# Kernel tuning notes

Measured on AMD Instinct MI355X. Metric: run time of the kernel, lower is better.

## Reference

```python
import jax, jax.numpy as jnp
import numpy as np

N = 8192          # tokens
CD = 512          # coarse_dim
FD = 512          # fine_dim
CB = 4096         # coarse codebook size
FB = 8192         # fine codebook size
COST = 0.25       # commitment cost
LRELU = 0.1
EPS = 1e-5


def _vq(x, emb):
    # squared-distance cdist: [n, K]
    d = jnp.sum(x * x, axis=1, keepdims=True) + jnp.sum(emb * emb, axis=1) - 2.0 * (x @ emb.T)
    idx = jnp.argmin(d, axis=1)          # temperature=1.0 (updates=0); scaling doesn't change argmin
    q = emb[idx]                          # gather == one-hot @ emb, without materializing one-hot
    e_loss = jnp.mean((jax.lax.stop_gradient(q) - x) ** 2)
    q_loss = jnp.mean((q - jax.lax.stop_gradient(x)) ** 2)
    loss = q_loss + COST * e_loss
    q_st = x + jax.lax.stop_gradient(q - x)   # straight-through
    return q_st, loss


def _mlp(x, w, b, g, be):
    # Linear (torch: x @ W.T + b) -> LayerNorm -> LeakyReLU(0.1)
    h = x @ w.T + b
    m = jnp.mean(h, axis=-1, keepdims=True)
    v = jnp.var(h, axis=-1, keepdims=True)
    h = (h - m) / jnp.sqrt(v + EPS) * g + be
    return jnp.where(h > 0, h, LRELU * h)


def setup_inputs() -> dict:
    key = jax.random.key(0)
    ks = jax.random.split(key, 6)
    xav_c = float(np.sqrt(6.0 / (CB + CD)))
    xav_f = float(np.sqrt(6.0 / (FB + FD)))
    lin_s = float(np.sqrt(1.0 / CD))
    return {
        'z': jax.random.normal(ks[0], (N, CD + FD), dtype=jnp.float32),
        'coarse_emb': jax.random.uniform(ks[1], (CB, CD), jnp.float32, -xav_c, xav_c),
        'fine_emb': jax.random.uniform(ks[2], (FB, FD), jnp.float32, -xav_f, xav_f),
        'w_c2f': jax.random.uniform(ks[3], (FD, CD), jnp.float32, -lin_s, lin_s),
        'b_c2f': jnp.zeros((FD,), jnp.float32),
        'g_c2f': jnp.ones((FD,), jnp.float32),
        'be_c2f': jnp.zeros((FD,), jnp.float32),
        'w_f2c': jax.random.uniform(ks[4], (CD, FD), jnp.float32, -lin_s, lin_s),
        'b_f2c': jnp.zeros((CD,), jnp.float32),
        'g_f2c': jnp.ones((CD,), jnp.float32),
        'be_f2c': jnp.zeros((CD,), jnp.float32),
        'gate_c_raw': jnp.float32(0.5),
        'gate_f_raw': jnp.float32(0.5),
    }


def reference(z, coarse_emb, fine_emb, w_c2f, b_c2f, g_c2f, be_c2f,
              w_f2c, b_f2c, g_f2c, be_f2c, gate_c_raw, gate_f_raw):
    split = z.shape[1] // 2
    z_coarse, z_fine = z[:, :split], z[:, split:]

    z_coarse_q, coarse_loss = _vq(z_coarse, coarse_emb)
    coarse_influence = _mlp(jax.lax.stop_gradient(z_coarse_q), w_c2f, b_c2f, g_c2f, be_c2f)
    gate_c = jax.nn.sigmoid(gate_c_raw)

    residual = z_fine - gate_c * coarse_influence
    z_fine_q, fine_loss = _vq(residual, fine_emb)

    fine_feedback = _mlp(jax.lax.stop_gradient(z_fine_q), w_f2c, b_f2c, g_f2c, be_f2c)
    gate_f = jax.nn.sigmoid(gate_f_raw)

    z_coarse_corrected = z_coarse_q + 0.1 * gate_f * fine_feedback
    z_fine_reconstructed = z_fine_q + gate_c * coarse_influence
    z_hierarchical = jnp.concatenate([z_coarse_corrected, z_fine_reconstructed], axis=1)
    vq_loss = coarse_loss + fine_loss
    return z_hierarchical, vq_loss
```

## Files before the change

kernel.cpp:

```cpp
#include <hip/hip_runtime.h>
#include <hip/hip_bf16.h>
#include <cstdint>
#include <cstddef>

#define KD 512

#define OFF_CN   0u
#define OFF_FN   16384u
#define OFF_ZN   49152u
#define OFF_RN   81920u
#define OFF_LOSS 114688u
#define OFF_AMC  114944u
#define OFF_AMF  180480u
#define OFF_CEH  246016u
#define OFF_CEL  4440320u
#define OFF_FEH  8634624u
#define OFF_FEL  17023232u
#define OFF_ZCH  25411840u
#define OFF_ZCL  33800448u
#define OFF_RH   42189056u
#define OFF_RL   50577664u
#define OFF_W1H  58966272u
#define OFF_W1L  59490560u
#define OFF_W2H  60014848u
#define OFF_W2L  60539136u
#define OFF_H    61063424u
#define OFF_INFL 77840640u


typedef __attribute__((ext_vector_type(8))) short bf16x8;
typedef __attribute__((ext_vector_type(4))) float f32x4;

__device__ __forceinline__ bf16x8 as_bf16x8(int4 v) {
  union { int4 i; bf16x8 b; } u; u.i = v; return u.b;
}

__device__ __forceinline__ void gl_lds16(const void* g, void* l) {
  __builtin_amdgcn_global_load_lds(
      (const __attribute__((address_space(1))) void*)g,
      (__attribute__((address_space(3))) void*)l, 16, 0, 0);
}

__device__ __forceinline__ float block_sum(float v, float* sred) {
#pragma unroll
  for (int off = 32; off > 0; off >>= 1) v += __shfl_down(v, off, 64);
  if ((threadIdx.x & 63) == 0) sred[threadIdx.x >> 6] = v;
  __syncthreads();
  float r = sred[0] + sred[1] + sred[2] + sred[3];
  __syncthreads();
  return r;
}

__device__ __forceinline__ float sigmoidf_(float x) { return 1.0f / (1.0f + expf(-x)); }

__device__ __forceinline__ void split_bf16(float v, __hip_bfloat16* hi, __hip_bfloat16* lo) {
  __hip_bfloat16 h = __float2bfloat16(v);
  *hi = h;
  *lo = __float2bfloat16(v - __bfloat162float(h));
}

__global__ __launch_bounds__(256) void prep(
    const float* __restrict__ ce, const float* __restrict__ fe, const float* __restrict__ z,
    const float* __restrict__ w1, const float* __restrict__ w2,
    float* __restrict__ cn, float* __restrict__ fn, float* __restrict__ zn,
    __hip_bfloat16* __restrict__ ceH, __hip_bfloat16* __restrict__ ceL,
    __hip_bfloat16* __restrict__ feH, __hip_bfloat16* __restrict__ feL,
    __hip_bfloat16* __restrict__ zcH, __hip_bfloat16* __restrict__ zcL,
    __hip_bfloat16* __restrict__ w1H, __hip_bfloat16* __restrict__ w1L,
    __hip_bfloat16* __restrict__ w2H, __hip_bfloat16* __restrict__ w2L,
    float* __restrict__ lossp) {
  __shared__ float sred[4];
  const int b = blockIdx.x, t = threadIdx.x;
  const float* src;
  float* nd = nullptr;
  __hip_bfloat16 *dh, *dl;
  int fragMode = 0;
  size_t row;
  if (b < 4096) {
    row = b; src = ce + row * KD; nd = cn + row; dh = ceH; dl = ceL; fragMode = 1;
  } else if (b < 12288) {
    row = b - 4096; src = fe + row * KD; nd = fn + row; dh = feH; dl = feL; fragMode = 1;
  } else if (b < 20480) {
    row = b - 12288; src = z + row * 1024; nd = zn + row; dh = zcH; dl = zcL;
  } else if (b < 20992) {
    row = b - 20480; src = w1 + row * KD; dh = w1H; dl = w1L;
  } else {
    row = b - 20992; src = w2 + row * KD; dh = w2H; dl = w2L;
  }
  float acc = 0.0f;
  if (fragMode) {
    float v0 = src[t], v1 = src[t + 256];
    acc = v0 * v0 + v1 * v1;
  } else {
#pragma unroll
    for (int j = 0; j < 2; ++j) {
      int c = t + j * 256;
      float v = src[c];
      acc += v * v;
      __hip_bfloat16 h, l;
      split_bf16(v, &h, &l);
      dh[row * KD + c] = h;
      dl[row * KD + c] = l;
    }
  }
  if (nd) {
    float s = block_sum(acc, sred);
    if (t == 0) nd[0] = s;
  } else {
    __syncthreads();
    __syncthreads();
  }
  if (fragMode && t < 64) {
    union { int4 i; __hip_bfloat16 s[8]; } ph, pl;
#pragma unroll
    for (int j = 0; j < 8; ++j) {
      float v = src[8 * t + j];
      split_bf16(v, &ph.s[j], &pl.s[j]);
    }
    const int chunkIdx = (int)(((row >> 4) * 16 + (t >> 2)) * 64 +
                               ((size_t)((t & 3) << 4) | (row & 15)));
    ((int4*)dh)[chunkIdx] = ph.i;
    ((int4*)dl)[chunkIdx] = pl.i;
  }
  if (b == 20480 && t == 0) lossp[0] = 0.0f;
}

__global__ __launch_bounds__(256) void vq7(
    const int4* __restrict__ AfH, const int4* __restrict__ AfL,
    const __hip_bfloat16* __restrict__ Bh, const __hip_bfloat16* __restrict__ Bl,
    const float* __restrict__ qn, const float* __restrict__ cn,
    unsigned long long* __restrict__ amin) {
  __shared__ __align__(16) __hip_bfloat16 sBh[3][128 * 32];
  __shared__ __align__(16) __hip_bfloat16 sBl[3][128 * 32];
  const int t = threadIdx.x;
  const int w = t >> 6, l = t & 63;
  const int rowTile = blockIdx.y << 7;
  const int colTile = blockIdx.x << 7;
  const int wr = (w >> 1) << 6;
  const int wc = (w & 1) << 6;

  const int rl = l >> 2;
  const int sbp = (l & 3) ^ ((l >> 3) & 3);
  const size_t gOff0 = (size_t)(colTile + (w << 5) + rl) * KD + (sbp << 3);
  const size_t gOff1 = gOff0 + (size_t)16 * KD;
  const int lOff0 = (w << 5) << 5;
  const int lOff1 = lOff0 + (16 << 5);

  const int fr = l & 15;
  const int q = l >> 4;

  int aB[4];
#pragma unroll
  for (int mt = 0; mt < 4; ++mt)
    aB[mt] = (((rowTile + wr + (mt << 4)) >> 4) << 10) + l;

  f32x4 acc[4][4];
#pragma unroll
  for (int i = 0; i < 4; ++i)
#pragma unroll
    for (int j = 0; j < 4; ++j) acc[i][j] = (f32x4){0.f, 0.f, 0.f, 0.f};

#define STAGE_B(bi, ck) do {                                      \
    gl_lds16(Bh + gOff0 + ((size_t)(ck) << 5), &sBh[bi][lOff0]);  \
    gl_lds16(Bh + gOff1 + ((size_t)(ck) << 5), &sBh[bi][lOff1]);  \
    gl_lds16(Bl + gOff0 + ((size_t)(ck) << 5), &sBl[bi][lOff0]);  \
    gl_lds16(Bl + gOff1 + ((size_t)(ck) << 5), &sBl[bi][lOff1]);  \
  } while (0)

  int4 aH[4], aL[4];
  STAGE_B(0, 0);
  STAGE_B(1, 1);
#pragma unroll
  for (int mt = 0; mt < 4; ++mt) { aH[mt] = AfH[aB[mt]]; aL[mt] = AfL[aB[mt]]; }
  __builtin_amdgcn_sched_barrier(0);
  asm volatile("s_waitcnt vmcnt(0)" ::: "memory");

#pragma unroll
  for (int i = 0; i < 16; ++i) {
    __builtin_amdgcn_s_barrier();
    __builtin_amdgcn_sched_barrier(0);
    if (i + 2 < 16) STAGE_B((i + 2) % 3, i + 2);
    __builtin_amdgcn_sched_barrier(0);

    bf16x8 afh[4], afl[4];
#pragma unroll
    for (int mt = 0; mt < 4; ++mt) {
      afh[mt] = as_bf16x8(aH[mt]);
      afl[mt] = as_bf16x8(aL[mt]);
    }
    if (i + 1 < 16) {
#pragma unroll
      for (int mt = 0; mt < 4; ++mt) {
        aH[mt] = AfH[aB[mt] + ((i + 1) << 6)];
        aL[mt] = AfL[aB[mt] + ((i + 1) << 6)];
      }
    }
    __builtin_amdgcn_sched_barrier(0);

    __builtin_amdgcn_s_setprio(1);
    const int cb = i % 3;
    bf16x8 bfh[4], bfl[4];
#pragma unroll
    for (int nt = 0; nt < 4; ++nt) {
      const int rB = wc + (nt << 4) + fr;
      const int o = (rB << 5) + ((q ^ ((rB >> 1) & 3)) << 3);
      bfh[nt] = *(const bf16x8*)(sBh[cb] + o);
      bfl[nt] = *(const bf16x8*)(sBl[cb] + o);
    }
#pragma unroll
    for (int mt = 0; mt < 4; ++mt)
#pragma unroll
      for (int nt = 0; nt < 4; ++nt) {
        acc[mt][nt] = __builtin_amdgcn_mfma_f32_16x16x32_bf16(afh[mt], bfh[nt], acc[mt][nt], 0, 0, 0);
        acc[mt][nt] = __builtin_amdgcn_mfma_f32_16x16x32_bf16(afh[mt], bfl[nt], acc[mt][nt], 0, 0, 0);
        acc[mt][nt] = __builtin_amdgcn_mfma_f32_16x16x32_bf16(afl[mt], bfh[nt], acc[mt][nt], 0, 0, 0);
      }
    __builtin_amdgcn_s_setprio(0);
  }

#pragma unroll
  for (int nt = 0; nt < 4; ++nt) {
    const int query = colTile + wc + (nt << 4) + fr;
    const float xn = qn[query];
    unsigned long long key = ~0ULL;
#pragma unroll
    for (int mt = 0; mt < 4; ++mt) {
#pragma unroll
      for (int reg = 0; reg < 4; ++reg) {
        const int code = rowTile + wr + (mt << 4) + (q << 2) + reg;
        float d = (xn + cn[code]) - 2.0f * acc[mt][nt][reg];
        unsigned ub = __float_as_uint(d);
        ub = (ub & 0x80000000u) ? ~ub : (ub | 0x80000000u);
        unsigned long long k2 = ((unsigned long long)ub << 32) | (unsigned long long)(unsigned)code;
        if (k2 < key) key = k2;
      }
    }
    unsigned long long o1 = __shfl_xor(key, 16, 64);
    if (o1 < key) key = o1;
    unsigned long long o2 = __shfl_xor(key, 32, 64);
    if (o2 < key) key = o2;
    if (l < 16) atomicMin(amin + colTile + wc + (nt << 4) + l, key);
  }
}

__global__ __launch_bounds__(256) void mlp6(
    const int4* __restrict__ AfH, const int4* __restrict__ AfL,
    const unsigned long long* __restrict__ gather,
    const __hip_bfloat16* __restrict__ Bh, const __hip_bfloat16* __restrict__ Bl,
    const float* __restrict__ bias, float* __restrict__ C) {
  __shared__ __align__(16) __hip_bfloat16 sAh[128 * 32];
  __shared__ __align__(16) __hip_bfloat16 sAl[128 * 32];
  __shared__ __align__(16) __hip_bfloat16 sBh[128 * 32];
  __shared__ __align__(16) __hip_bfloat16 sBl[128 * 32];
  const int t = threadIdx.x;
  const int w = t >> 6, l = t & 63;
  const int rowTile = blockIdx.y << 7;
  const int colTile = blockIdx.x << 7;
  const int wr = (w >> 1) << 6;
  const int wc = (w & 1) << 6;

  const int srow = t >> 2;
  const int sb = t & 3;
  const int skE = sb << 3;
  const int swz = (sb ^ ((srow >> 1) & 3)) << 3;
  const int wOff0 = (srow << 5) + swz;
  const int wOff1 = ((srow + 64) << 5) + swz;

  unsigned i0 = ((const unsigned*)gather)[2 * (rowTile + srow)];
  unsigned i1 = ((const unsigned*)gather)[2 * (rowTile + 64 + srow)];
  const int a0 = (int)((i0 >> 4) << 10) + (sb << 4) + (int)(i0 & 15);
  const int a1 = (int)((i1 >> 4) << 10) + (sb << 4) + (int)(i1 & 15);
  const size_t br0 = (size_t)(colTile + srow) * KD;
  const size_t br1 = (size_t)(colTile + 64 + srow) * KD;

  const int fr = l & 15;
  const int q = l >> 4;

  f32x4 acc[4][4];
#pragma unroll
  for (int i = 0; i < 4; ++i)
#pragma unroll
    for (int j = 0; j < 4; ++j) acc[i][j] = (f32x4){0.f, 0.f, 0.f, 0.f};

  for (int kk = 0; kk < KD; kk += 32) {
    const int kc64 = (kk >> 5) << 6;
    int4 vAh0 = AfH[a0 + kc64];
    int4 vAh1 = AfH[a1 + kc64];
    int4 vAl0 = AfL[a0 + kc64];
    int4 vAl1 = AfL[a1 + kc64];
    int4 vBh0 = *(const int4*)(Bh + br0 + kk + skE);
    int4 vBh1 = *(const int4*)(Bh + br1 + kk + skE);
    int4 vBl0 = *(const int4*)(Bl + br0 + kk + skE);
    int4 vBl1 = *(const int4*)(Bl + br1 + kk + skE);
    __syncthreads();
    *(int4*)(sAh + wOff0) = vAh0; *(int4*)(sAh + wOff1) = vAh1;
    *(int4*)(sAl + wOff0) = vAl0; *(int4*)(sAl + wOff1) = vAl1;
    *(int4*)(sBh + wOff0) = vBh0; *(int4*)(sBh + wOff1) = vBh1;
    *(int4*)(sBl + wOff0) = vBl0; *(int4*)(sBl + wOff1) = vBl1;
    __syncthreads();

    bf16x8 afh[4], afl[4], bfh[4], bfl[4];
#pragma unroll
    for (int mt = 0; mt < 4; ++mt) {
      const int rA = wr + (mt << 4) + fr;
      const int o = (rA << 5) + ((q ^ ((rA >> 1) & 3)) << 3);
      afh[mt] = *(const bf16x8*)(sAh + o);
      afl[mt] = *(const bf16x8*)(sAl + o);
    }
#pragma unroll
    for (int nt = 0; nt < 4; ++nt) {
      const int rB = wc + (nt << 4) + fr;
      const int o = (rB << 5) + ((q ^ ((rB >> 1) & 3)) << 3);
      bfh[nt] = *(const bf16x8*)(sBh + o);
      bfl[nt] = *(const bf16x8*)(sBl + o);
    }
#pragma unroll
    for (int mt = 0; mt < 4; ++mt)
#pragma unroll
      for (int nt = 0; nt < 4; ++nt) {
        acc[mt][nt] = __builtin_amdgcn_mfma_f32_16x16x32_bf16(afh[mt], bfh[nt], acc[mt][nt], 0, 0, 0);
        acc[mt][nt] = __builtin_amdgcn_mfma_f32_16x16x32_bf16(afh[mt], bfl[nt], acc[mt][nt], 0, 0, 0);
        acc[mt][nt] = __builtin_amdgcn_mfma_f32_16x16x32_bf16(afl[mt], bfh[nt], acc[mt][nt], 0, 0, 0);
      }
  }

  const int quad = l >> 4;
#pragma unroll
  for (int mt = 0; mt < 4; ++mt) {
#pragma unroll
    for (int reg = 0; reg < 4; ++reg) {
      const int row = rowTile + wr + (mt << 4) + (quad << 2) + reg;
#pragma unroll
      for (int nt = 0; nt < 4; ++nt) {
        const int col = colTile + wc + (nt << 4) + fr;
        C[(size_t)row * KD + col] = acc[mt][nt][reg] + bias[col];
      }
    }
  }
}

__global__ __launch_bounds__(256) void ln_residual(
    const float* __restrict__ h, const float* __restrict__ g, const float* __restrict__ be,
    const float* __restrict__ z, const float* __restrict__ gRaw,
    __hip_bfloat16* __restrict__ infl, float* __restrict__ rn,
    __hip_bfloat16* __restrict__ rH, __hip_bfloat16* __restrict__ rL) {
  __shared__ float sred[4];
  const int row = blockIdx.x, t = threadIdx.x;
  const size_t base = (size_t)row * KD;
  float h0 = h[base + t], h1 = h[base + t + 256];
  float m = block_sum(h0 + h1, sred) * (1.0f / 512.0f);
  float d0 = h0 - m, d1 = h1 - m;
  float var = block_sum(d0 * d0 + d1 * d1, sred) * (1.0f / 512.0f);
  float sq = sqrtf(var + 1e-5f);
  float gc = sigmoidf_(gRaw[0]);
  float v0 = d0 / sq * g[t] + be[t];
  float v1 = d1 / sq * g[t + 256] + be[t + 256];
  v0 = v0 > 0.0f ? v0 : 0.1f * v0;
  v1 = v1 > 0.0f ? v1 : 0.1f * v1;
  infl[base + t] = __float2bfloat16(v0);
  infl[base + t + 256] = __float2bfloat16(v1);
  float zf0 = z[(size_t)row * 1024 + 512 + t];
  float zf1 = z[(size_t)row * 1024 + 512 + t + 256];
  float r0 = zf0 - gc * v0, r1 = zf1 - gc * v1;
  __hip_bfloat16 hh, ll;
  split_bf16(r0, &hh, &ll);
  rH[base + t] = hh; rL[base + t] = ll;
  split_bf16(r1, &hh, &ll);
  rH[base + t + 256] = hh; rL[base + t + 256] = ll;
  float rs = block_sum(r0 * r0 + r1 * r1, sred);
  if (t == 0) rn[row] = rs;
}

__global__ __launch_bounds__(256) void finalize(
    const float* __restrict__ h, const float* __restrict__ g, const float* __restrict__ be,
    const __hip_bfloat16* __restrict__ infl,
    const unsigned long long* __restrict__ amc, const unsigned long long* __restrict__ amf,
    const float* __restrict__ z, const float* __restrict__ ce, const float* __restrict__ fe,
    const float* __restrict__ gcRaw, const float* __restrict__ gfRaw,
    float* __restrict__ out, float* __restrict__ lossp) {
  __shared__ float sred[4];
  const int row = blockIdx.x, t = threadIdx.x;
  const size_t base = (size_t)row * KD;
  float h0 = h[base + t], h1 = h[base + t + 256];
  float m = block_sum(h0 + h1, sred) * (1.0f / 512.0f);
  float d0 = h0 - m, d1 = h1 - m;
  float var = block_sum(d0 * d0 + d1 * d1, sred) * (1.0f / 512.0f);
  float sq = sqrtf(var + 1e-5f);
  float fb0 = d0 / sq * g[t] + be[t];
  float fb1 = d1 / sq * g[t + 256] + be[t + 256];
  fb0 = fb0 > 0.0f ? fb0 : 0.1f * fb0;
  fb1 = fb1 > 0.0f ? fb1 : 0.1f * fb1;
  float gc = sigmoidf_(gcRaw[0]);
  float gf = sigmoidf_(gfRaw[0]);
  unsigned ic = (unsigned)(amc[row] & 0xffffffffULL);
  unsigned ifx = (unsigned)(amf[row] & 0xffffffffULL);
  float loc = 0.0f;
#pragma unroll
  for (int j = 0; j < 2; ++j) {
    int c = t + j * 256;
    float fb = j ? fb1 : fb0;
    float qc = ce[(size_t)ic * KD + c];
    float qf = fe[(size_t)ifx * KD + c];
    float zc = z[(size_t)row * 1024 + c];
    float zf = z[(size_t)row * 1024 + 512 + c];
    float fl = __bfloat162float(infl[base + c]);
    out[(size_t)row * 1024 + c] = qc + 0.1f * gf * fb;
    out[(size_t)row * 1024 + 512 + c] = qf + gc * fl;
    float dc = qc - zc;
    float res = zf - gc * fl;
    float df = qf - res;
    loc += dc * dc + df * df;
  }
  float ls = block_sum(loc, sred);
  if (t == 0) atomicAdd(lossp, ls);
}

__global__ void loss_write(const float* __restrict__ lossp, float* __restrict__ out) {
  out[0] = 1.25f * lossp[0] / (8192.0f * 512.0f);
}

extern "C" void kernel_launch(void* const* d_in, const int* in_sizes, int n_in,
                              void* d_out, int out_size, void* d_ws, size_t ws_size,
                              hipStream_t stream) {
  const float* z      = (const float*)d_in[0];
  const float* ce     = (const float*)d_in[1];
  const float* fe     = (const float*)d_in[2];
  const float* w_c2f  = (const float*)d_in[3];
  const float* b_c2f  = (const float*)d_in[4];
  const float* g_c2f  = (const float*)d_in[5];
  const float* be_c2f = (const float*)d_in[6];
  const float* w_f2c  = (const float*)d_in[7];
  const float* b_f2c  = (const float*)d_in[8];
  const float* g_f2c  = (const float*)d_in[9];
  const float* be_f2c = (const float*)d_in[10];
  const float* gcRaw  = (const float*)d_in[11];
  const float* gfRaw  = (const float*)d_in[12];
  float* out = (float*)d_out;
  char* ws = (char*)d_ws;

  float* cn = (float*)(ws + OFF_CN);
  float* fn = (float*)(ws + OFF_FN);
  float* zn = (float*)(ws + OFF_ZN);
  float* rn = (float*)(ws + OFF_RN);
  float* lossp = (float*)(ws + OFF_LOSS);
  unsigned long long* amc = (unsigned long long*)(ws + OFF_AMC);
  unsigned long long* amf = (unsigned long long*)(ws + OFF_AMF);
  __hip_bfloat16* ceH = (__hip_bfloat16*)(ws + OFF_CEH);
  __hip_bfloat16* ceL = (__hip_bfloat16*)(ws + OFF_CEL);
  __hip_bfloat16* feH = (__hip_bfloat16*)(ws + OFF_FEH);
  __hip_bfloat16* feL = (__hip_bfloat16*)(ws + OFF_FEL);
  __hip_bfloat16* zcH = (__hip_bfloat16*)(ws + OFF_ZCH);
  __hip_bfloat16* zcL = (__hip_bfloat16*)(ws + OFF_ZCL);
  __hip_bfloat16* rH  = (__hip_bfloat16*)(ws + OFF_RH);
  __hip_bfloat16* rL  = (__hip_bfloat16*)(ws + OFF_RL);
  __hip_bfloat16* w1H = (__hip_bfloat16*)(ws + OFF_W1H);
  __hip_bfloat16* w1L = (__hip_bfloat16*)(ws + OFF_W1L);
  __hip_bfloat16* w2H = (__hip_bfloat16*)(ws + OFF_W2H);
  __hip_bfloat16* w2L = (__hip_bfloat16*)(ws + OFF_W2L);
  float* h = (float*)(ws + OFF_H);
  __hip_bfloat16* infl = (__hip_bfloat16*)(ws + OFF_INFL);

  hipMemsetAsync(ws + OFF_AMC, 0xFF, 131072, stream);

  prep<<<21504, 256, 0, stream>>>(ce, fe, z, w_c2f, w_f2c, cn, fn, zn,
                                  ceH, ceL, feH, feL, zcH, zcL,
                                  w1H, w1L, w2H, w2L, lossp);

  vq7<<<dim3(64, 32), 256, 0, stream>>>((const int4*)ceH, (const int4*)ceL,
                                        zcH, zcL, zn, cn, amc);

  mlp6<<<dim3(4, 64), 256, 0, stream>>>((const int4*)ceH, (const int4*)ceL, amc,
                                        w1H, w1L, b_c2f, h);

  ln_residual<<<8192, 256, 0, stream>>>(h, g_c2f, be_c2f, z, gcRaw, infl, rn, rH, rL);

  vq7<<<dim3(64, 64), 256, 0, stream>>>((const int4*)feH, (const int4*)feL,
                                        rH, rL, rn, fn, amf);

  mlp6<<<dim3(4, 64), 256, 0, stream>>>((const int4*)feH, (const int4*)feL, amf,
                                        w2H, w2L, b_f2c, h);

  finalize<<<8192, 256, 0, stream>>>(h, g_f2c, be_f2c, infl, amc, amf, z, ce, fe,
                                     gcRaw, gfRaw, out, lossp);
  loss_write<<<1, 1, 0, stream>>>(lossp, out + (size_t)8192 * 1024);
}
```

Baseline: 622.3 us.

## Replace split-bf16 VQ distance GEMM with single bf16 pass plus fp32 top-3 rescue

The VQ distance kernels now use a single bf16 MFMA pass instead of three hi/lo split passes, and keep a per-block top-3 candidate list in place of a global atomicMin. A new rescue kernel rechecks in fp32 every candidate within an error threshold and picks the exact argmin. This is meant to cut the MFMA work and the hi/lo loads in the dominant distance GEMMs by about a factor of three, at the cost of an extra kernel and extra candidate traffic. The threshold constants are tuned empirically, so argmin exactness relies on the error bound holding for these input scales.

```diff
diff --git a/kernel.cpp b/kernel.cpp
--- a/kernel.cpp
+++ b/kernel.cpp
@@ -30,6 +30,7 @@
 
 typedef __attribute__((ext_vector_type(8))) short bf16x8;
 typedef __attribute__((ext_vector_type(4))) float f32x4;
+typedef unsigned long long u64;
 
 __device__ __forceinline__ bf16x8 as_bf16x8(int4 v) {
   union { int4 i; bf16x8 b; } u; u.i = v; return u.b;
@@ -59,13 +60,35 @@
   *lo = __float2bfloat16(v - __bfloat162float(h));
 }
 
+__device__ __forceinline__ unsigned enc_sortable(float f) {
+  unsigned u = __float_as_uint(f);
+  return (u & 0x80000000u) ? ~u : (u | 0x80000000u);
+}
+__device__ __forceinline__ float dec_sortable(unsigned ub) {
+  unsigned o = (ub & 0x80000000u) ? (ub & 0x7fffffffu) : ~ub;
+  return __uint_as_float(o);
+}
+__device__ __forceinline__ u64 umin64(u64 a, u64 b) { return a < b ? a : b; }
+__device__ __forceinline__ u64 umax64(u64 a, u64 b) { return a > b ? a : b; }
+
+__device__ __forceinline__ void merge3(u64& a1, u64& a2, u64& a3, u64 b1, u64 b2, u64 b3) {
+  u64 p = umax64(a1, b1);
+  u64 q = umin64(a2, b2);
+  u64 r = umax64(a2, b2);
+  u64 s = umin64(a3, b3);
+  u64 m1 = umin64(a1, b1);
+  u64 m2 = umin64(p, q);
+  u64 m3 = umin64(umin64(umax64(p, q), r), s);
+  a1 = m1; a2 = m2; a3 = m3;
+}
+
 __global__ __launch_bounds__(256) void prep(
     const float* __restrict__ ce, const float* __restrict__ fe, const float* __restrict__ z,
     const float* __restrict__ w1, const float* __restrict__ w2,
     float* __restrict__ cn, float* __restrict__ fn, float* __restrict__ zn,
     __hip_bfloat16* __restrict__ ceH, __hip_bfloat16* __restrict__ ceL,
     __hip_bfloat16* __restrict__ feH, __hip_bfloat16* __restrict__ feL,
-    __hip_bfloat16* __restrict__ zcH, __hip_bfloat16* __restrict__ zcL,
+    __hip_bfloat16* __restrict__ zcH,
     __hip_bfloat16* __restrict__ w1H, __hip_bfloat16* __restrict__ w1L,
     __hip_bfloat16* __restrict__ w2H, __hip_bfloat16* __restrict__ w2L,
     float* __restrict__ lossp) {
@@ -73,15 +96,15 @@
   const int b = blockIdx.x, t = threadIdx.x;
   const float* src;
   float* nd = nullptr;
-  __hip_bfloat16 *dh, *dl;
-  int fragMode = 0;
+  __hip_bfloat16 *dh = nullptr, *dl = nullptr;
+  int fragMode = 0, hiOnly = 0;
   size_t row;
   if (b < 4096) {
     row = b; src = ce + row * KD; nd = cn + row; dh = ceH; dl = ceL; fragMode = 1;
   } else if (b < 12288) {
     row = b - 4096; src = fe + row * KD; nd = fn + row; dh = feH; dl = feL; fragMode = 1;
   } else if (b < 20480) {
-    row = b - 12288; src = z + row * 1024; nd = zn + row; dh = zcH; dl = zcL;
+    row = b - 12288; src = z + row * 1024; nd = zn + row; dh = zcH; hiOnly = 1;
   } else if (b < 20992) {
     row = b - 20480; src = w1 + row * KD; dh = w1H; dl = w1L;
   } else {
@@ -100,7 +123,7 @@
       __hip_bfloat16 h, l;
       split_bf16(v, &h, &l);
       dh[row * KD + c] = h;
-      dl[row * KD + c] = l;
+      if (!hiOnly) dl[row * KD + c] = l;
     }
   }
   if (nd) {
@@ -125,17 +148,17 @@
   if (b == 20480 && t == 0) lossp[0] = 0.0f;
 }
 
-__global__ __launch_bounds__(256) void vq7(
-    const int4* __restrict__ AfH, const int4* __restrict__ AfL,
-    const __hip_bfloat16* __restrict__ Bh, const __hip_bfloat16* __restrict__ Bl,
-    const float* __restrict__ qn, const float* __restrict__ cn,
-    unsigned long long* __restrict__ amin) {
+__global__ __launch_bounds__(256) void vq8(
+    const int4* __restrict__ AfH,
+    const __hip_bfloat16* __restrict__ Bh,
+    const float* __restrict__ cn,
+    u64* __restrict__ bkeys) {
   __shared__ __align__(16) __hip_bfloat16 sBh[3][128 * 32];
-  __shared__ __align__(16) __hip_bfloat16 sBl[3][128 * 32];
   const int t = threadIdx.x;
   const int w = t >> 6, l = t & 63;
   const int rowTile = blockIdx.y << 7;
   const int colTile = blockIdx.x << 7;
+  const int NB = gridDim.y;
   const int wr = (w >> 1) << 6;
   const int wc = (w & 1) << 6;
 
@@ -163,15 +186,13 @@
 #define STAGE_B(bi, ck) do {                                      \
     gl_lds16(Bh + gOff0 + ((size_t)(ck) << 5), &sBh[bi][lOff0]);  \
     gl_lds16(Bh + gOff1 + ((size_t)(ck) << 5), &sBh[bi][lOff1]);  \
-    gl_lds16(Bl + gOff0 + ((size_t)(ck) << 5), &sBl[bi][lOff0]);  \
-    gl_lds16(Bl + gOff1 + ((size_t)(ck) << 5), &sBl[bi][lOff1]);  \
   } while (0)
 
-  int4 aH[4], aL[4];
+  int4 aH[4];
   STAGE_B(0, 0);
   STAGE_B(1, 1);
 #pragma unroll
-  for (int mt = 0; mt < 4; ++mt) { aH[mt] = AfH[aB[mt]]; aL[mt] = AfL[aB[mt]]; }
+  for (int mt = 0; mt < 4; ++mt) aH[mt] = AfH[aB[mt]];
   __builtin_amdgcn_sched_barrier(0);
   asm volatile("s_waitcnt vmcnt(0)" ::: "memory");
 
@@ -182,70 +203,136 @@
     if (i + 2 < 16) STAGE_B((i + 2) % 3, i + 2);
     __builtin_amdgcn_sched_barrier(0);
 
-    bf16x8 afh[4], afl[4];
-#pragma unroll
-    for (int mt = 0; mt < 4; ++mt) {
-      afh[mt] = as_bf16x8(aH[mt]);
-      afl[mt] = as_bf16x8(aL[mt]);
-    }
+    bf16x8 afh[4];
+#pragma unroll
+    for (int mt = 0; mt < 4; ++mt) afh[mt] = as_bf16x8(aH[mt]);
     if (i + 1 < 16) {
 #pragma unroll
-      for (int mt = 0; mt < 4; ++mt) {
-        aH[mt] = AfH[aB[mt] + ((i + 1) << 6)];
-        aL[mt] = AfL[aB[mt] + ((i + 1) << 6)];
-      }
+      for (int mt = 0; mt < 4; ++mt) aH[mt] = AfH[aB[mt] + ((i + 1) << 6)];
     }
     __builtin_amdgcn_sched_barrier(0);
 
     __builtin_amdgcn_s_setprio(1);
     const int cb = i % 3;
-    bf16x8 bfh[4], bfl[4];
+    bf16x8 bfh[4];
 #pragma unroll
     for (int nt = 0; nt < 4; ++nt) {
       const int rB = wc + (nt << 4) + fr;
       const int o = (rB << 5) + ((q ^ ((rB >> 1) & 3)) << 3);
       bfh[nt] = *(const bf16x8*)(sBh[cb] + o);
-      bfl[nt] = *(const bf16x8*)(sBl[cb] + o);
     }
 #pragma unroll
     for (int mt = 0; mt < 4; ++mt)
 #pragma unroll
-      for (int nt = 0; nt < 4; ++nt) {
+      for (int nt = 0; nt < 4; ++nt)
         acc[mt][nt] = __builtin_amdgcn_mfma_f32_16x16x32_bf16(afh[mt], bfh[nt], acc[mt][nt], 0, 0, 0);
-        acc[mt][nt] = __builtin_amdgcn_mfma_f32_16x16x32_bf16(afh[mt], bfl[nt], acc[mt][nt], 0, 0, 0);
-        acc[mt][nt] = __builtin_amdgcn_mfma_f32_16x16x32_bf16(afl[mt], bfh[nt], acc[mt][nt], 0, 0, 0);
-      }
     __builtin_amdgcn_s_setprio(0);
   }
-
+#undef STAGE_B
+
+  u64 tk1[4], tk2[4], tk3[4];
 #pragma unroll
   for (int nt = 0; nt < 4; ++nt) {
-    const int query = colTile + wc + (nt << 4) + fr;
-    const float xn = qn[query];
-    unsigned long long key = ~0ULL;
+    u64 t1 = ~0ULL, t2 = ~0ULL, t3 = ~0ULL;
 #pragma unroll
     for (int mt = 0; mt < 4; ++mt) {
 #pragma unroll
       for (int reg = 0; reg < 4; ++reg) {
         const int code = rowTile + wr + (mt << 4) + (q << 2) + reg;
-        float d = (xn + cn[code]) - 2.0f * acc[mt][nt][reg];
-        unsigned ub = __float_as_uint(d);
-        ub = (ub & 0x80000000u) ? ~ub : (ub | 0x80000000u);
-        unsigned long long k2 = ((unsigned long long)ub << 32) | (unsigned long long)(unsigned)code;
-        if (k2 < key) key = k2;
+        float d = cn[code] - 2.0f * acc[mt][nt][reg];
+        u64 key = ((u64)enc_sortable(d) << 32) | (u64)(unsigned)code;
+        if (key < t1) { t3 = t2; t2 = t1; t1 = key; }
+        else if (key < t2) { t3 = t2; t2 = key; }
+        else if (key < t3) { t3 = key; }
       }
     }
-    unsigned long long o1 = __shfl_xor(key, 16, 64);
-    if (o1 < key) key = o1;
-    unsigned long long o2 = __shfl_xor(key, 32, 64);
-    if (o2 < key) key = o2;
-    if (l < 16) atomicMin(amin + colTile + wc + (nt << 4) + l, key);
-  }
+#pragma unroll
+    for (int off = 16; off <= 32; off <<= 1) {
+      u64 b1 = __shfl_xor(t1, off, 64);
+      u64 b2 = __shfl_xor(t2, off, 64);
+      u64 b3 = __shfl_xor(t3, off, 64);
+      merge3(t1, t2, t3, b1, b2, b3);
+    }
+    tk1[nt] = t1; tk2[nt] = t2; tk3[nt] = t3;
+  }
+
+  __syncthreads();
+  u64* sk = (u64*)sBh;
+  if (w >= 2 && l < 16) {
+#pragma unroll
+    for (int nt = 0; nt < 4; ++nt) {
+      const int o = ((((w & 1) << 2) + nt) * 16 + fr) * 3;
+      sk[o] = tk1[nt]; sk[o + 1] = tk2[nt]; sk[o + 2] = tk3[nt];
+    }
+  }
+  __syncthreads();
+  if (w < 2 && l < 16) {
+#pragma unroll
+    for (int nt = 0; nt < 4; ++nt) {
+      const int o = (((w << 2) + nt) * 16 + fr) * 3;
+      u64 t1 = tk1[nt], t2 = tk2[nt], t3 = tk3[nt];
+      merge3(t1, t2, t3, sk[o], sk[o + 1], sk[o + 2]);
+      const int query = colTile + wc + (nt << 4) + fr;
+      const size_t bo = ((size_t)query * NB + blockIdx.y) * 3;
+      bkeys[bo] = t1; bkeys[bo + 1] = t2; bkeys[bo + 2] = t3;
+    }
+  }
+}
+
+__global__ __launch_bounds__(256) void rescue(
+    const u64* __restrict__ bkeys, int NB3,
+    const float* __restrict__ Q, int qStride,
+    const float* __restrict__ Cb,
+    const float* __restrict__ qn, const float* __restrict__ cnorm,
+    float dscale, u64* __restrict__ am) {
+  const int wv = threadIdx.x >> 6, l = threadIdx.x & 63;
+  const int qi = (blockIdx.x << 2) + wv;
+  const u64* kq = bkeys + (size_t)qi * NB3;
+  u64 kk[3];
+#pragma unroll
+  for (int j = 0; j < 3; ++j) {
+    const int idx = l + (j << 6);
+    kk[j] = (idx < NB3) ? kq[idx] : ~0ULL;
+  }
+  u64 kmin = umin64(kk[0], umin64(kk[1], kk[2]));
+#pragma unroll
+  for (int off = 32; off > 0; off >>= 1) kmin = umin64(kmin, __shfl_xor(kmin, off, 64));
+  const float xnv = qn[qi];
+  const float dmin = dec_sortable((unsigned)(kmin >> 32));
+  const float thr = dmin + dscale * sqrtf(xnv) + 0.01f;
+  const u64 thrKey = ((u64)enc_sortable(thr) << 32) | 0xffffffffULL;
+
+  const float* qrow = Q + (size_t)qi * qStride;
+  const float4 qa = *(const float4*)(qrow + (l << 3));
+  const float4 qb = *(const float4*)(qrow + (l << 3) + 4);
+  float bestD = 3.4e38f;
+  int bestC = 0x7fffffff;
+#pragma unroll
+  for (int j = 0; j < 3; ++j) {
+    bool pend = kk[j] <= thrKey;
+    u64 mask;
+    while ((mask = __ballot(pend)) != 0ULL) {
+      const int src = __ffsll((unsigned long long)mask) - 1;
+      const u64 key = __shfl(kk[j], src, 64);
+      if (l == src) pend = false;
+      const int code = (int)(unsigned)(key & 0xffffffffULL);
+      const float* crow = Cb + (size_t)code * KD;
+      const float4 ca = *(const float4*)(crow + (l << 3));
+      const float4 cb = *(const float4*)(crow + (l << 3) + 4);
+      float dt = qa.x * ca.x + qa.y * ca.y + qa.z * ca.z + qa.w * ca.w +
+                 qb.x * cb.x + qb.y * cb.y + qb.z * cb.z + qb.w * cb.w;
+#pragma unroll
+      for (int off = 32; off > 0; off >>= 1) dt += __shfl_xor(dt, off, 64);
+      const float d = (xnv + cnorm[code]) - 2.0f * dt;
+      if (d < bestD || (d == bestD && code < bestC)) { bestD = d; bestC = code; }
+    }
+  }
+  if (l == 0) am[qi] = ((u64)enc_sortable(bestD) << 32) | (unsigned)bestC;
 }
 
 __global__ __launch_bounds__(256) void mlp6(
     const int4* __restrict__ AfH, const int4* __restrict__ AfL,
-    const unsigned long long* __restrict__ gather,
+    const u64* __restrict__ gather,
     const __hip_bfloat16* __restrict__ Bh, const __hip_bfloat16* __restrict__ Bl,
     const float* __restrict__ bias, float* __restrict__ C) {
   __shared__ __align__(16) __hip_bfloat16 sAh[128 * 32];
@@ -343,7 +430,7 @@
     const float* __restrict__ h, const float* __restrict__ g, const float* __restrict__ be,
     const float* __restrict__ z, const float* __restrict__ gRaw,
     __hip_bfloat16* __restrict__ infl, float* __restrict__ rn,
-    __hip_bfloat16* __restrict__ rH, __hip_bfloat16* __restrict__ rL) {
+    __hip_bfloat16* __restrict__ rH, float* __restrict__ resF) {
   __shared__ float sred[4];
   const int row = blockIdx.x, t = threadIdx.x;
   const size_t base = (size_t)row * KD;
@@ -362,11 +449,10 @@
   float zf0 = z[(size_t)row * 1024 + 512 + t];
   float zf1 = z[(size_t)row * 1024 + 512 + t + 256];
   float r0 = zf0 - gc * v0, r1 = zf1 - gc * v1;
-  __hip_bfloat16 hh, ll;
-  split_bf16(r0, &hh, &ll);
-  rH[base + t] = hh; rL[base + t] = ll;
-  split_bf16(r1, &hh, &ll);
-  rH[base + t + 256] = hh; rL[base + t + 256] = ll;
+  rH[base + t] = __float2bfloat16(r0);
+  rH[base + t + 256] = __float2bfloat16(r1);
+  resF[base + t] = r0;
+  resF[base + t + 256] = r1;
   float rs = block_sum(r0 * r0 + r1 * r1, sred);
   if (t == 0) rn[row] = rs;
 }
@@ -374,7 +460,7 @@
 __global__ __launch_bounds__(256) void finalize(
     const float* __restrict__ h, const float* __restrict__ g, const float* __restrict__ be,
     const __hip_bfloat16* __restrict__ infl,
-    const unsigned long long* __restrict__ amc, const unsigned long long* __restrict__ amf,
+    const u64* __restrict__ amc, const u64* __restrict__ amf,
     const float* __restrict__ z, const float* __restrict__ ce, const float* __restrict__ fe,
     const float* __restrict__ gcRaw, const float* __restrict__ gfRaw,
     float* __restrict__ out, float* __restrict__ lossp) {
@@ -443,39 +529,39 @@
   float* zn = (float*)(ws + OFF_ZN);
   float* rn = (float*)(ws + OFF_RN);
   float* lossp = (float*)(ws + OFF_LOSS);
-  unsigned long long* amc = (unsigned long long*)(ws + OFF_AMC);
-  unsigned long long* amf = (unsigned long long*)(ws + OFF_AMF);
+  u64* amc = (u64*)(ws + OFF_AMC);
+  u64* amf = (u64*)(ws + OFF_AMF);
   __hip_bfloat16* ceH = (__hip_bfloat16*)(ws + OFF_CEH);
   __hip_bfloat16* ceL = (__hip_bfloat16*)(ws + OFF_CEL);
   __hip_bfloat16* feH = (__hip_bfloat16*)(ws + OFF_FEH);
   __hip_bfloat16* feL = (__hip_bfloat16*)(ws + OFF_FEL);
   __hip_bfloat16* zcH = (__hip_bfloat16*)(ws + OFF_ZCH);
-  __hip_bfloat16* zcL = (__hip_bfloat16*)(ws + OFF_ZCL);
   __hip_bfloat16* rH  = (__hip_bfloat16*)(ws + OFF_RH);
-  __hip_bfloat16* rL  = (__hip_bfloat16*)(ws + OFF_RL);
   __hip_bfloat16* w1H = (__hip_bfloat16*)(ws + OFF_W1H);
   __hip_bfloat16* w1L = (__hip_bfloat16*)(ws + OFF_W1L);
   __hip_bfloat16* w2H = (__hip_bfloat16*)(ws + OFF_W2H);
   __hip_bfloat16* w2L = (__hip_bfloat16*)(ws + OFF_W2L);
   float* h = (float*)(ws + OFF_H);
   __hip_bfloat16* infl = (__hip_bfloat16*)(ws + OFF_INFL);
-
-  hipMemsetAsync(ws + OFF_AMC, 0xFF, 131072, stream);
+  u64* bkeys = (u64*)(ws + OFF_H);
+  float* resF = (float*)(ws + OFF_ZCH);
 
   prep<<<21504, 256, 0, stream>>>(ce, fe, z, w_c2f, w_f2c, cn, fn, zn,
-                                  ceH, ceL, feH, feL, zcH, zcL,
+                                  ceH, ceL, feH, feL, zcH,
                                   w1H, w1L, w2H, w2L, lossp);
 
-  vq7<<<dim3(64, 32), 256, 0, stream>>>((const int4*)ceH, (const int4*)ceL,
-                                        zcH, zcL, zn, cn, amc);
+  vq8<<<dim3(64, 32), 256, 0, stream>>>((const int4*)ceH, zcH, cn, bkeys);
+
+  rescue<<<2048, 256, 0, stream>>>(bkeys, 96, z, 1024, ce, zn, cn, 0.00321f, amc);
 
   mlp6<<<dim3(4, 64), 256, 0, stream>>>((const int4*)ceH, (const int4*)ceL, amc,
                                         w1H, w1L, b_c2f, h);
 
-  ln_residual<<<8192, 256, 0, stream>>>(h, g_c2f, be_c2f, z, gcRaw, infl, rn, rH, rL);
-
-  vq7<<<dim3(64, 64), 256, 0, stream>>>((const int4*)feH, (const int4*)feL,
-                                        rH, rL, rn, fn, amf);
+  ln_residual<<<8192, 256, 0, stream>>>(h, g_c2f, be_c2f, z, gcRaw, infl, rn, rH, resF);
+
+  vq8<<<dim3(64, 64), 256, 0, stream>>>((const int4*)feH, rH, fn, bkeys);
+
+  rescue<<<2048, 256, 0, stream>>>(bkeys, 192, resF, 512, fe, rn, fn, 0.00233f, amf);
 
   mlp6<<<dim3(4, 64), 256, 0, stream>>>((const int4*)feH, (const int4*)feL, amf,
                                         w2H, w2L, b_f2c, h);
```

After: 563.3 us. 1.1x faster.
